# Performance work log

Hardware: AMD Instinct MI355X
Metric: run time of the kernel (lower is better)

## Reference

```python
import jax, jax.numpy as jnp
import numpy as np

B, N_WAY, N_SHOT, QUERY, NUM_SLOT, D = 64, 5, 5, 15, 8, 640
LAMBDA = 0.1
NEG_INF = jnp.float32(-1e30)


def cover_select(scores):
    # scores: [b, n_way, num_slot]. For each class in order, greedily pick the
    # highest-scoring slot not already taken (replicates torch sort+dedup loop).
    def per_batch(s):
        def step(taken, row):
            sel = jnp.argmax(jnp.where(taken, NEG_INF, row))
            return taken.at[sel].set(True), sel
        _, sel = jax.lax.scan(step, jnp.zeros(s.shape[-1], dtype=bool), s)
        return sel  # [n_way]
    return jax.vmap(per_batch)(scores)  # [b, n_way]


def euclid(gallery, query):
    # gallery [b, n, d], query [b, m, d] -> [b, m, n]
    return jnp.sum((query[:, :, None, :] - gallery[:, None, :, :]) ** 2, axis=-1)


def loss_acc(proto, q, labels_query):
    diff = euclid(proto, q)                                   # [b, n_way*query, n_way]
    logits = jax.nn.log_softmax(-diff, axis=2)
    logits = logits.reshape(B, QUERY, N_WAY, N_WAY)
    nll = -jnp.take_along_axis(logits, labels_query, axis=3).mean()
    y_hat = jnp.argmax(logits, axis=3)
    acc = (y_hat == labels_query[..., 0]).astype(jnp.float32).mean()
    return nll, acc


def setup_inputs() -> dict:
    key = jax.random.key(0)
    k0, k1, k2, k3 = jax.random.split(key, 4)
    n_total = B * N_WAY * (N_SHOT + QUERY)
    out_f = jax.random.normal(k0, (n_total, NUM_SLOT, D), dtype=jnp.float32)
    labels_support = jax.random.randint(k1, (B, N_SHOT, N_WAY, 1), 0, N_WAY, dtype=jnp.int32)
    labels_query = jax.random.randint(k2, (B, QUERY, N_WAY, 1), 0, N_WAY, dtype=jnp.int32)
    att_loss = jax.random.uniform(k3, (1,), dtype=jnp.float32)
    return {"out_f": out_f, "labels_support": labels_support,
            "labels_query": labels_query, "att_loss": att_loss}


def reference(out_f, labels_support, labels_query, att_loss):
    # mode == 'train' path of SimilarityLoss.forward
    b, d = B, out_f.shape[-1]
    ns = b * N_WAY * N_SHOT
    # class prototypes over shots: [b*n_way, num_slot, d]
    sup = out_f[:ns].reshape(b * N_WAY, N_SHOT, NUM_SLOT, d).mean(1)
    qry = out_f[ns:].reshape(b, N_WAY, QUERY, NUM_SLOT, d)

    max_s = cover_select(sup.mean(-1).reshape(b, N_WAY, NUM_SLOT))  # [b, n_way]

    sup_b = sup.reshape(b, N_WAY, NUM_SLOT, d)
    # proto[j, c] = sup_b[j, c, max_s[j, c]]
    proto = jax.vmap(jax.vmap(lambda s, i: s[i]))(sup_b, max_s)     # [b, n_way, d]

    # get_selected path: each class's queries pick that class's selected slot
    out_query = jax.vmap(jax.vmap(lambda q, i: q[:, i, :]))(qry, max_s)  # [b, n_way, query, d]
    out_query = out_query.reshape(b, N_WAY * QUERY, d)

    # get_22 path (faithful to the original non-reset record_temp accumulation):
    # for image s, pick among rows {q22[j, s', max_s[j, i]] : s' <= s, i < n_way}
    # the row with the largest mean over d.
    imgs = N_WAY * QUERY
    q22 = qry.reshape(b, imgs, NUM_SLOT, d)
    cand = jax.vmap(lambda q, i: q[:, i, :])(q22, max_s)            # [b, imgs, n_way, d]
    L = imgs * N_WAY
    m = cand.mean(-1).reshape(b, L)                                 # flat order (s, i)
    prefix = jnp.arange(L)[None, :] < ((jnp.arange(imgs) + 1) * N_WAY)[:, None]  # [imgs, L]
    k = jnp.argmax(jnp.where(prefix[None], m[:, None, :], NEG_INF), axis=-1)     # [b, imgs]
    out_query_t = jnp.take_along_axis(cand.reshape(b, L, d), k[:, :, None], axis=1)  # [b, imgs, d]

    nll, acc = loss_acc(proto, out_query, labels_query)
    loss = nll + jnp.float32(LAMBDA) * att_loss[0]
    loss_t, acc_t = loss_acc(proto, out_query_t, labels_query)
    return (loss, loss_t, acc, acc_t)
```

## Files before the change

kernel.cpp:

```cpp
#include <hip/hip_runtime.h>

#define BB 64
#define N_WAY 5
#define N_SHOT 5
#define QUERY 15
#define NUM_SLOT 8
#define DD 640
#define IMGS (N_WAY * QUERY)
#define NS (BB * N_WAY * N_SHOT)
#define NROWS 6400
#define ROWSZ (NUM_SLOT * DD)
#define F4_PER_SLOT 160
#define NELEM (BB * IMGS)
#define NGROUP (BB * N_WAY)
#define PIECES 19
#define NBLK (BB * PIECES)

__global__ __launch_bounds__(256) void k_pass1(const float* __restrict__ out_f,
                                               float* __restrict__ rowmean,
                                               float* __restrict__ proto_all,
                                               float* __restrict__ pn2_all) {
    int b = blockIdx.x;
    int t = threadIdx.x;
    int slot = t >> 5;
    int l = t & 31;
    if (b < NGROUP) {
        const int g = b;
        float4 acc[5];
        #pragma unroll
        for (int k = 0; k < 5; ++k) acc[k] = make_float4(0.f, 0.f, 0.f, 0.f);
        #pragma unroll
        for (int sh = 0; sh < N_SHOT; ++sh) {
            const float4* p = (const float4*)(out_f +
                ((size_t)((g * N_SHOT + sh) * NUM_SLOT + slot)) * DD);
            float s = 0.f;
            #pragma unroll
            for (int k = 0; k < 5; ++k) {
                float4 v = p[l + k * 32];
                acc[k].x += v.x; acc[k].y += v.y; acc[k].z += v.z; acc[k].w += v.w;
                s += (v.x + v.y) + (v.z + v.w);
            }
            #pragma unroll
            for (int off = 16; off; off >>= 1) s += __shfl_down(s, off, 32);
            if (l == 0) rowmean[(g * N_SHOT + sh) * NUM_SLOT + slot] = s * (1.f / DD);
        }
        float4* pp = (float4*)(proto_all + ((size_t)(g * NUM_SLOT + slot)) * DD);
        float ssq = 0.f;
        #pragma unroll
        for (int k = 0; k < 5; ++k) {
            acc[k].x *= 0.2f; acc[k].y *= 0.2f; acc[k].z *= 0.2f; acc[k].w *= 0.2f;
            pp[l + k * 32] = acc[k];
            ssq += acc[k].x * acc[k].x + acc[k].y * acc[k].y
                 + acc[k].z * acc[k].z + acc[k].w * acc[k].w;
        }
        #pragma unroll
        for (int off = 16; off; off >>= 1) ssq += __shfl_down(ssq, off, 32);
        if (l == 0) pn2_all[g * NUM_SLOT + slot] = ssq;
    } else {
        int r = NS + (b - NGROUP);
        const float4* p = (const float4*)(out_f + (size_t)r * ROWSZ) + slot * F4_PER_SLOT;
        float s = 0.f;
        #pragma unroll
        for (int k = 0; k < 5; ++k) {
            float4 v = p[l + k * 32];
            s += (v.x + v.y) + (v.z + v.w);
        }
        #pragma unroll
        for (int off = 16; off; off >>= 1) s += __shfl_down(s, off, 32);
        if (l == 0) rowmean[r * NUM_SLOT + slot] = s * (1.f / DD);
    }
}

__global__ __launch_bounds__(256) void k_mid(const float* __restrict__ out_f,
                                             const float* __restrict__ rowmean,
                                             const float* __restrict__ proto_all,
                                             const float* __restrict__ pn2_all,
                                             const int* __restrict__ labels_query,
                                             float4* __restrict__ part) {
    int b = blockIdx.x;
    int j = b / PIECES, piece = b - j * PIECES;
    int t = threadIdx.x;
    int wave = t >> 6, lane = t & 63;
    int m = piece * 4 + wave;

    __shared__ float qbt[NUM_SLOT][76];
    __shared__ float supm[N_WAY * NUM_SLOT];
    __shared__ int   msS[N_WAY];
    __shared__ float4 redS[4];

    const float* qbase = rowmean + (size_t)(NS + j * IMGS) * NUM_SLOT;
    if (t < 150) {
        float4 v = ((const float4*)qbase)[t];
        int s = t >> 1, sl0 = (t & 1) * 4;
        qbt[sl0 + 0][s] = v.x; qbt[sl0 + 1][s] = v.y;
        qbt[sl0 + 2][s] = v.z; qbt[sl0 + 3][s] = v.w;
    }
    if (t >= 192 && t < 192 + N_WAY * NUM_SLOT) {
        int idx = t - 192;
        int c = idx >> 3, s = idx & 7;
        const float* sb = rowmean + (size_t)j * (N_WAY * N_SHOT * NUM_SLOT)
                          + c * (N_SHOT * NUM_SLOT) + s;
        supm[idx] = (sb[0] + sb[8] + sb[16] + sb[24] + sb[32]) * 0.2f;
    }
    __syncthreads();

    if (t == 0) {
        unsigned taken = 0u;
        #pragma unroll
        for (int c = 0; c < N_WAY; ++c) {
            float best = -3.0e38f; int bi = 0;
            #pragma unroll
            for (int s = 0; s < NUM_SLOT; ++s) {
                float v = supm[c * NUM_SLOT + s];
                if (!((taken >> s) & 1u) && v > best) { best = v; bi = s; }
            }
            taken |= (1u << bi);
            msS[c] = bi;
        }
    }
    __syncthreads();

    int ms[N_WAY];
    #pragma unroll
    for (int n = 0; n < N_WAY; ++n) ms[n] = msS[n];

    float2 pv[N_WAY][5];
    float p2r[N_WAY];
    #pragma unroll
    for (int n = 0; n < N_WAY; ++n) {
        const float2* pp = (const float2*)(proto_all +
            ((size_t)((j * N_WAY + n) * NUM_SLOT + ms[n])) * DD) + lane * 5;
        #pragma unroll
        for (int k = 0; k < 5; ++k) pv[n][k] = pp[k];
        p2r[n] = pn2_all[(j * N_WAY + n) * NUM_SLOT + ms[n]];
    }

    float4 lv = make_float4(0.f, 0.f, 0.f, 0.f);
    if (m < IMGS) {
        const float2* q1p = (const float2*)(out_f +
            (size_t)(NS + j * IMGS + m) * ROWSZ + ms[m / QUERY] * DD) + lane * 5;
        float2 q1v[5];
        #pragma unroll
        for (int k = 0; k < 5; ++k) q1v[k] = q1p[k];

        float bv = -3.0e38f; int bi = 0x7fffffff;
        #pragma unroll
        for (int rep = 0; rep < 2; ++rep) {
            int s = lane + rep * 64;
            if (s <= m) {
                #pragma unroll
                for (int c = 0; c < N_WAY; ++c) {
                    float x = qbt[ms[c]][s];
                    int flat = s * N_WAY + c;
                    if (x > bv || (x == bv && flat < bi)) { bv = x; bi = flat; }
                }
            }
        }
        #pragma unroll
        for (int off = 32; off; off >>= 1) {
            float ov = __shfl_down(bv, off, 64);
            int   oi = __shfl_down(bi, off, 64);
            if (ov > bv || (ov == bv && oi < bi)) { bv = ov; bi = oi; }
        }
        bi = __shfl(bi, 0, 64);

        int s2 = bi / N_WAY, c2 = bi - s2 * N_WAY;
        const float2* q2p = (const float2*)(out_f +
            (size_t)(NS + j * IMGS + s2) * ROWSZ + ms[c2] * DD) + lane * 5;
        float2 q2v[5];
        #pragma unroll
        for (int k = 0; k < 5; ++k) q2v[k] = q2p[k];

        float s1[N_WAY] = {0, 0, 0, 0, 0};
        float s2a[N_WAY] = {0, 0, 0, 0, 0};
        #pragma unroll
        for (int n = 0; n < N_WAY; ++n) {
            #pragma unroll
            for (int k = 0; k < 5; ++k) {
                s1[n]  += q1v[k].x * pv[n][k].x + q1v[k].y * pv[n][k].y;
                s2a[n] += q2v[k].x * pv[n][k].x + q2v[k].y * pv[n][k].y;
            }
        }
        #pragma unroll
        for (int n = 0; n < N_WAY; ++n) {
            #pragma unroll
            for (int off = 32; off; off >>= 1) {
                s1[n]  += __shfl_down(s1[n],  off, 64);
                s2a[n] += __shfl_down(s2a[n], off, 64);
            }
        }
        if (lane == 0) {
            int label = labels_query[j * IMGS + m];
            {
                float li[N_WAY]; float mx = -3.0e38f;
                #pragma unroll
                for (int n = 0; n < N_WAY; ++n) { li[n] = 2.f * s1[n] - p2r[n]; mx = fmaxf(mx, li[n]); }
                float se = 0.f;
                #pragma unroll
                for (int n = 0; n < N_WAY; ++n) se += expf(li[n] - mx);
                float lse = mx + logf(se);
                int bn = 0; float bvv = li[0];
                #pragma unroll
                for (int n = 1; n < N_WAY; ++n) if (li[n] > bvv) { bvv = li[n]; bn = n; }
                lv.x = -(li[label] - lse);
                lv.z = (bn == label) ? 1.f : 0.f;
            }
            {
                float li[N_WAY]; float mx = -3.0e38f;
                #pragma unroll
                for (int n = 0; n < N_WAY; ++n) { li[n] = 2.f * s2a[n] - p2r[n]; mx = fmaxf(mx, li[n]); }
                float se = 0.f;
                #pragma unroll
                for (int n = 0; n < N_WAY; ++n) se += expf(li[n] - mx);
                float lse = mx + logf(se);
                int bn = 0; float bvv = li[0];
                #pragma unroll
                for (int n = 1; n < N_WAY; ++n) if (li[n] > bvv) { bvv = li[n]; bn = n; }
                lv.y = -(li[label] - lse);
                lv.w = (bn == label) ? 1.f : 0.f;
            }
        }
    }
    if (lane == 0) redS[wave] = lv;
    __syncthreads();
    if (t == 0) {
        float4 s0 = redS[0], s1 = redS[1], s2 = redS[2], s3 = redS[3];
        part[b] = make_float4(s0.x + s1.x + s2.x + s3.x,
                              s0.y + s1.y + s2.y + s3.y,
                              s0.z + s1.z + s2.z + s3.z,
                              s0.w + s1.w + s2.w + s3.w);
    }
}

__global__ __launch_bounds__(256) void k_final(const float4* __restrict__ part,
                                               const float* __restrict__ att_loss,
                                               float* __restrict__ out) {
    __shared__ float4 red[256];
    int t = threadIdx.x;
    float4 s = make_float4(0.f, 0.f, 0.f, 0.f);
    for (int i = t; i < NBLK; i += 256) {
        float4 v = part[i];
        s.x += v.x; s.y += v.y; s.z += v.z; s.w += v.w;
    }
    red[t] = s;
    __syncthreads();
    for (int w = 128; w; w >>= 1) {
        if (t < w) {
            red[t].x += red[t + w].x; red[t].y += red[t + w].y;
            red[t].z += red[t + w].z; red[t].w += red[t + w].w;
        }
        __syncthreads();
    }
    if (t == 0) {
        out[0] = red[0].x / (float)NELEM + 0.1f * att_loss[0];
        out[1] = red[0].y / (float)NELEM;
        out[2] = red[0].z / (float)NELEM;
        out[3] = red[0].w / (float)NELEM;
    }
}

extern "C" void kernel_launch(void* const* d_in, const int* in_sizes, int n_in,
                              void* d_out, int out_size, void* d_ws, size_t ws_size,
                              hipStream_t stream) {
    const float* out_f        = (const float*)d_in[0];
    const int*   labels_query = (const int*)d_in[2];
    const float* att_loss     = (const float*)d_in[3];
    float* out = (float*)d_out;

    float*  rowmean   = (float*)d_ws;
    float*  proto_all = rowmean + NROWS * NUM_SLOT;
    float*  pn2_all   = proto_all + NGROUP * NUM_SLOT * DD;
    float4* part      = (float4*)(pn2_all + NGROUP * NUM_SLOT);

    k_pass1<<<NGROUP + NELEM, 256, 0, stream>>>(out_f, rowmean, proto_all, pn2_all);
    k_mid<<<NBLK, 256, 0, stream>>>(out_f, rowmean, proto_all, pn2_all,
                                    labels_query, part);
    k_final<<<1, 256, 0, stream>>>(part, att_loss, out);
}
```

Measured before the change: 39.16 us.

## Share selected prototypes via LDS across 8 waves and precompute support slot means

Each k_mid block now runs 512 threads (8 waves, 10 pieces per batch) and stages the five selected prototype slices once in shared memory, instead of every wave loading them into registers from global memory. k_pass1 computes the per-slot support means directly from the averaged prototype and stores them, which removes the per-shot row-mean reductions and their stores. The aim is to cut redundant global prototype loads, shuffle reductions and register pressure. The cost is an extra barrier, a strided LDS fill loop, and larger blocks with fewer blocks overall.

```diff
diff --git a/kernel.cpp b/kernel.cpp
--- a/kernel.cpp
+++ b/kernel.cpp
@@ -8,18 +8,19 @@
 #define DD 640
 #define IMGS (N_WAY * QUERY)
 #define NS (BB * N_WAY * N_SHOT)
-#define NROWS 6400
+#define QROWS (BB * IMGS)
 #define ROWSZ (NUM_SLOT * DD)
 #define F4_PER_SLOT 160
 #define NELEM (BB * IMGS)
 #define NGROUP (BB * N_WAY)
-#define PIECES 19
+#define PIECES 10
 #define NBLK (BB * PIECES)
 
 __global__ __launch_bounds__(256) void k_pass1(const float* __restrict__ out_f,
-                                               float* __restrict__ rowmean,
+                                               float* __restrict__ rowmean_q,
                                                float* __restrict__ proto_all,
-                                               float* __restrict__ pn2_all) {
+                                               float* __restrict__ pn2_all,
+                                               float* __restrict__ supm_g) {
     int b = blockIdx.x;
     int t = threadIdx.x;
     int slot = t >> 5;
@@ -33,32 +34,35 @@
         for (int sh = 0; sh < N_SHOT; ++sh) {
             const float4* p = (const float4*)(out_f +
                 ((size_t)((g * N_SHOT + sh) * NUM_SLOT + slot)) * DD);
-            float s = 0.f;
             #pragma unroll
             for (int k = 0; k < 5; ++k) {
                 float4 v = p[l + k * 32];
                 acc[k].x += v.x; acc[k].y += v.y; acc[k].z += v.z; acc[k].w += v.w;
-                s += (v.x + v.y) + (v.z + v.w);
-            }
-            #pragma unroll
-            for (int off = 16; off; off >>= 1) s += __shfl_down(s, off, 32);
-            if (l == 0) rowmean[(g * N_SHOT + sh) * NUM_SLOT + slot] = s * (1.f / DD);
+            }
         }
         float4* pp = (float4*)(proto_all + ((size_t)(g * NUM_SLOT + slot)) * DD);
-        float ssq = 0.f;
+        float ssq = 0.f, sm = 0.f;
         #pragma unroll
         for (int k = 0; k < 5; ++k) {
             acc[k].x *= 0.2f; acc[k].y *= 0.2f; acc[k].z *= 0.2f; acc[k].w *= 0.2f;
             pp[l + k * 32] = acc[k];
             ssq += acc[k].x * acc[k].x + acc[k].y * acc[k].y
                  + acc[k].z * acc[k].z + acc[k].w * acc[k].w;
-        }
-        #pragma unroll
-        for (int off = 16; off; off >>= 1) ssq += __shfl_down(ssq, off, 32);
-        if (l == 0) pn2_all[g * NUM_SLOT + slot] = ssq;
+            sm  += (acc[k].x + acc[k].y) + (acc[k].z + acc[k].w);
+        }
+        #pragma unroll
+        for (int off = 16; off; off >>= 1) {
+            ssq += __shfl_down(ssq, off, 32);
+            sm  += __shfl_down(sm,  off, 32);
+        }
+        if (l == 0) {
+            pn2_all[g * NUM_SLOT + slot] = ssq;
+            supm_g[g * NUM_SLOT + slot]  = sm * (1.f / DD);
+        }
     } else {
-        int r = NS + (b - NGROUP);
-        const float4* p = (const float4*)(out_f + (size_t)r * ROWSZ) + slot * F4_PER_SLOT;
+        int rq = b - NGROUP;
+        const float4* p = (const float4*)(out_f + (size_t)(NS + rq) * ROWSZ)
+                          + slot * F4_PER_SLOT;
         float s = 0.f;
         #pragma unroll
         for (int k = 0; k < 5; ++k) {
@@ -67,41 +71,39 @@
         }
         #pragma unroll
         for (int off = 16; off; off >>= 1) s += __shfl_down(s, off, 32);
-        if (l == 0) rowmean[r * NUM_SLOT + slot] = s * (1.f / DD);
-    }
-}
-
-__global__ __launch_bounds__(256) void k_mid(const float* __restrict__ out_f,
-                                             const float* __restrict__ rowmean,
+        if (l == 0) rowmean_q[rq * NUM_SLOT + slot] = s * (1.f / DD);
+    }
+}
+
+__global__ __launch_bounds__(512) void k_mid(const float* __restrict__ out_f,
+                                             const float* __restrict__ rowmean_q,
                                              const float* __restrict__ proto_all,
                                              const float* __restrict__ pn2_all,
+                                             const float* __restrict__ supm_g,
                                              const int* __restrict__ labels_query,
                                              float4* __restrict__ part) {
     int b = blockIdx.x;
     int j = b / PIECES, piece = b - j * PIECES;
     int t = threadIdx.x;
     int wave = t >> 6, lane = t & 63;
-    int m = piece * 4 + wave;
-
-    __shared__ float qbt[NUM_SLOT][76];
-    __shared__ float supm[N_WAY * NUM_SLOT];
+    int m = piece * 8 + wave;
+
+    __shared__ float qbt[NUM_SLOT][80];
+    __shared__ float supmS[N_WAY * NUM_SLOT];
     __shared__ int   msS[N_WAY];
-    __shared__ float4 redS[4];
-
-    const float* qbase = rowmean + (size_t)(NS + j * IMGS) * NUM_SLOT;
+    __shared__ float p2S[N_WAY];
+    __shared__ __align__(16) float2 protoS[N_WAY * 5][64];
+    __shared__ float4 redS[8];
+
+    const float* qbase = rowmean_q + (size_t)j * IMGS * NUM_SLOT;
     if (t < 150) {
         float4 v = ((const float4*)qbase)[t];
         int s = t >> 1, sl0 = (t & 1) * 4;
         qbt[sl0 + 0][s] = v.x; qbt[sl0 + 1][s] = v.y;
         qbt[sl0 + 2][s] = v.z; qbt[sl0 + 3][s] = v.w;
     }
-    if (t >= 192 && t < 192 + N_WAY * NUM_SLOT) {
-        int idx = t - 192;
-        int c = idx >> 3, s = idx & 7;
-        const float* sb = rowmean + (size_t)j * (N_WAY * N_SHOT * NUM_SLOT)
-                          + c * (N_SHOT * NUM_SLOT) + s;
-        supm[idx] = (sb[0] + sb[8] + sb[16] + sb[24] + sb[32]) * 0.2f;
-    }
+    if (t >= 160 && t < 160 + N_WAY * NUM_SLOT)
+        supmS[t - 160] = supm_g[j * (N_WAY * NUM_SLOT) + (t - 160)];
     __syncthreads();
 
     if (t == 0) {
@@ -111,7 +113,7 @@
             float best = -3.0e38f; int bi = 0;
             #pragma unroll
             for (int s = 0; s < NUM_SLOT; ++s) {
-                float v = supm[c * NUM_SLOT + s];
+                float v = supmS[c * NUM_SLOT + s];
                 if (!((taken >> s) & 1u) && v > best) { best = v; bi = s; }
             }
             taken |= (1u << bi);
@@ -123,26 +125,26 @@
     int ms[N_WAY];
     #pragma unroll
     for (int n = 0; n < N_WAY; ++n) ms[n] = msS[n];
-
-    float2 pv[N_WAY][5];
-    float p2r[N_WAY];
-    #pragma unroll
-    for (int n = 0; n < N_WAY; ++n) {
-        const float2* pp = (const float2*)(proto_all +
-            ((size_t)((j * N_WAY + n) * NUM_SLOT + ms[n])) * DD) + lane * 5;
-        #pragma unroll
-        for (int k = 0; k < 5; ++k) pv[n][k] = pp[k];
-        p2r[n] = pn2_all[(j * N_WAY + n) * NUM_SLOT + ms[n]];
-    }
-
-    float4 lv = make_float4(0.f, 0.f, 0.f, 0.f);
+    if (t < N_WAY) p2S[t] = pn2_all[(j * N_WAY + t) * NUM_SLOT + ms[t]];
+
+    float2 q1v[5];
     if (m < IMGS) {
         const float2* q1p = (const float2*)(out_f +
             (size_t)(NS + j * IMGS + m) * ROWSZ + ms[m / QUERY] * DD) + lane * 5;
-        float2 q1v[5];
         #pragma unroll
         for (int k = 0; k < 5; ++k) q1v[k] = q1p[k];
-
+    }
+
+    for (int idx = t; idx < N_WAY * 320; idx += 512) {
+        int n = idx / 320, r = idx - n * 320;
+        int lane_d = r / 5, k = r - lane_d * 5;
+        const float2* gp = (const float2*)(proto_all +
+            ((size_t)((j * N_WAY + n) * NUM_SLOT + ms[n])) * DD);
+        protoS[n * 5 + k][lane_d] = gp[r];
+    }
+
+    float2 q2v[5];
+    if (m < IMGS) {
         float bv = -3.0e38f; int bi = 0x7fffffff;
         #pragma unroll
         for (int rep = 0; rep < 2; ++rep) {
@@ -163,22 +165,25 @@
             if (ov > bv || (ov == bv && oi < bi)) { bv = ov; bi = oi; }
         }
         bi = __shfl(bi, 0, 64);
-
         int s2 = bi / N_WAY, c2 = bi - s2 * N_WAY;
         const float2* q2p = (const float2*)(out_f +
             (size_t)(NS + j * IMGS + s2) * ROWSZ + ms[c2] * DD) + lane * 5;
-        float2 q2v[5];
         #pragma unroll
         for (int k = 0; k < 5; ++k) q2v[k] = q2p[k];
-
+    }
+    __syncthreads();
+
+    float4 lv = make_float4(0.f, 0.f, 0.f, 0.f);
+    if (m < IMGS) {
         float s1[N_WAY] = {0, 0, 0, 0, 0};
         float s2a[N_WAY] = {0, 0, 0, 0, 0};
         #pragma unroll
         for (int n = 0; n < N_WAY; ++n) {
             #pragma unroll
             for (int k = 0; k < 5; ++k) {
-                s1[n]  += q1v[k].x * pv[n][k].x + q1v[k].y * pv[n][k].y;
-                s2a[n] += q2v[k].x * pv[n][k].x + q2v[k].y * pv[n][k].y;
+                float2 p = protoS[n * 5 + k][lane];
+                s1[n]  += q1v[k].x * p.x + q1v[k].y * p.y;
+                s2a[n] += q2v[k].x * p.x + q2v[k].y * p.y;
             }
         }
         #pragma unroll
@@ -194,7 +199,7 @@
             {
                 float li[N_WAY]; float mx = -3.0e38f;
                 #pragma unroll
-                for (int n = 0; n < N_WAY; ++n) { li[n] = 2.f * s1[n] - p2r[n]; mx = fmaxf(mx, li[n]); }
+                for (int n = 0; n < N_WAY; ++n) { li[n] = 2.f * s1[n] - p2S[n]; mx = fmaxf(mx, li[n]); }
                 float se = 0.f;
                 #pragma unroll
                 for (int n = 0; n < N_WAY; ++n) se += expf(li[n] - mx);
@@ -208,7 +213,7 @@
             {
                 float li[N_WAY]; float mx = -3.0e38f;
                 #pragma unroll
-                for (int n = 0; n < N_WAY; ++n) { li[n] = 2.f * s2a[n] - p2r[n]; mx = fmaxf(mx, li[n]); }
+                for (int n = 0; n < N_WAY; ++n) { li[n] = 2.f * s2a[n] - p2S[n]; mx = fmaxf(mx, li[n]); }
                 float se = 0.f;
                 #pragma unroll
                 for (int n = 0; n < N_WAY; ++n) se += expf(li[n] - mx);
@@ -224,11 +229,12 @@
     if (lane == 0) redS[wave] = lv;
     __syncthreads();
     if (t == 0) {
-        float4 s0 = redS[0], s1 = redS[1], s2 = redS[2], s3 = redS[3];
-        part[b] = make_float4(s0.x + s1.x + s2.x + s3.x,
-                              s0.y + s1.y + s2.y + s3.y,
-                              s0.z + s1.z + s2.z + s3.z,
-                              s0.w + s1.w + s2.w + s3.w);
+        float4 s = redS[0];
+        #pragma unroll
+        for (int w = 1; w < 8; ++w) {
+            s.x += redS[w].x; s.y += redS[w].y; s.z += redS[w].z; s.w += redS[w].w;
+        }
+        part[b] = s;
     }
 }
 
@@ -267,13 +273,15 @@
     const float* att_loss     = (const float*)d_in[3];
     float* out = (float*)d_out;
 
-    float*  rowmean   = (float*)d_ws;
-    float*  proto_all = rowmean + NROWS * NUM_SLOT;
+    float*  rowmean_q = (float*)d_ws;
+    float*  proto_all = rowmean_q + QROWS * NUM_SLOT;
     float*  pn2_all   = proto_all + NGROUP * NUM_SLOT * DD;
-    float4* part      = (float4*)(pn2_all + NGROUP * NUM_SLOT);
-
-    k_pass1<<<NGROUP + NELEM, 256, 0, stream>>>(out_f, rowmean, proto_all, pn2_all);
-    k_mid<<<NBLK, 256, 0, stream>>>(out_f, rowmean, proto_all, pn2_all,
-                                    labels_query, part);
+    float*  supm_g    = pn2_all + NGROUP * NUM_SLOT;
+    float4* part      = (float4*)(supm_g + NGROUP * NUM_SLOT);
+
+    k_pass1<<<NGROUP + QROWS, 256, 0, stream>>>(out_f, rowmean_q, proto_all,
+                                                pn2_all, supm_g);
+    k_mid<<<NBLK, 512, 0, stream>>>(out_f, rowmean_q, proto_all, pn2_all,
+                                    supm_g, labels_query, part);
     k_final<<<1, 256, 0, stream>>>(part, att_loss, out);
 }
```

New measurement: 42.47 us. 8.5% more time.
